# Optimization experiments

Hardware: AMD Instinct MI355X
Metric: run time of the kernel (lower is better)

## Reference

```python
import jax, jax.numpy as jnp
import numpy as np

B, S, D, H = 4, 2048, 1024, 16
HD = D // H
SCALE = HD ** -0.5

def setup_inputs() -> dict:
    key = jax.random.key(0)
    k1, k2, k3 = jax.random.split(key, 3)
    x = jax.random.normal(k1, (B, S, D), dtype=jnp.float32)
    W_qkv = jax.random.normal(k2, (D, 3 * D), dtype=jnp.float32) * (D ** -0.5)
    b_qkv = jnp.zeros((3 * D,), dtype=jnp.float32)
    W_proj = jax.random.normal(k3, (D, D), dtype=jnp.float32) * (D ** -0.5)
    b_proj = jnp.zeros((D,), dtype=jnp.float32)
    return {"x": x, "W_qkv": W_qkv, "b_qkv": b_qkv, "W_proj": W_proj, "b_proj": b_proj}

def reference(x, W_qkv, b_qkv, W_proj, b_proj):
    # x: [B,S,D] -> qkv: [B,S,3D] -> [3,B,H,S,hd]
    qkv = x @ W_qkv + b_qkv
    qkv = qkv.reshape(B, S, 3, H, HD).transpose(2, 0, 3, 1, 4)
    q, k, v = qkv[0], qkv[1], qkv[2]
    # naive full attention: [B,H,S,S]
    attn = jnp.einsum('bhqd,bhkd->bhqk', q, k) * SCALE
    attn = jax.nn.softmax(attn, axis=-1)
    out = jnp.einsum('bhqk,bhkd->bhqd', attn, v)
    out = out.transpose(0, 2, 1, 3).reshape(B, S, D)
    return out @ W_proj + b_proj
```

## Files before the change

### kernel.cpp

```cpp
#include <hip/hip_runtime.h>

typedef __bf16 bf16x8 __attribute__((ext_vector_type(8)));
typedef unsigned short ushort8 __attribute__((ext_vector_type(8)));
typedef float floatx4 __attribute__((ext_vector_type(4)));
typedef unsigned int uintx4 __attribute__((ext_vector_type(4)));

__device__ __forceinline__ unsigned short f2bf(float f) {
  unsigned int u = __builtin_bit_cast(unsigned int, f);
  u += 0x7fffu + ((u >> 16) & 1u);
  return (unsigned short)(u >> 16);
}
__device__ __forceinline__ unsigned int pkbf(float a, float b) {
  unsigned int r;
  asm("v_cvt_pk_bf16_f32 %0, %1, %2" : "=v"(r) : "v"(a), "v"(b));
  return r;
}
__device__ __forceinline__ floatx4 MFMA16(bf16x8 a, bf16x8 b, floatx4 c) {
  return __builtin_amdgcn_mfma_f32_16x16x32_bf16(a, b, c, 0, 0, 0);
}

#define GLOAD16(gsrc, ldst)                                                  \
  __builtin_amdgcn_global_load_lds(                                          \
      (const __attribute__((address_space(1))) void*)(gsrc),                 \
      (__attribute__((address_space(3))) void*)(ldst), 16, 0, 0)

__global__ __launch_bounds__(256) void fill_f32(
    float* __restrict__ out, float val, size_t n) {
  const size_t t = (size_t)blockIdx.x * 256 + threadIdx.x;
  for (size_t i = t; i < n; i += (size_t)gridDim.x * 256) out[i] = val;
}

__global__ __launch_bounds__(256) void cvt_f32_bf16(
    const float* __restrict__ in, unsigned short* __restrict__ out) {
  const size_t t = (size_t)blockIdx.x * 256 + threadIdx.x;
  const float4 a = ((const float4*)in)[2 * t];
  const float4 b = ((const float4*)in)[2 * t + 1];
  uintx4 u;
  u[0] = pkbf(a.x, a.y); u[1] = pkbf(a.z, a.w);
  u[2] = pkbf(b.x, b.y); u[3] = pkbf(b.z, b.w);
  *(uintx4*)&out[t * 8] = u;
}

__global__ __launch_bounds__(256) void transpose_w(
    const float* __restrict__ in, unsigned short* __restrict__ out, int C) {
  __shared__ float T[64][65];
  const int tid = threadIdx.x;
  const int r0 = blockIdx.y * 64, c0 = blockIdx.x * 64;
#pragma unroll
  for (int e = 0; e < 4; ++e) {
    const int idx = e * 256 + tid;
    const int row = idx >> 4, cg = idx & 15;
    const float4 f = *(const float4*)&in[(size_t)(r0 + row) * C + c0 + cg * 4];
    T[row][cg * 4] = f.x; T[row][cg * 4 + 1] = f.y;
    T[row][cg * 4 + 2] = f.z; T[row][cg * 4 + 3] = f.w;
  }
  __syncthreads();
#pragma unroll
  for (int e = 0; e < 2; ++e) {
    const int idx = e * 256 + tid;
    const int cc = idx >> 3, rg = idx & 7;
    uintx4 u;
#pragma unroll
    for (int k = 0; k < 4; ++k)
      u[k] = pkbf(T[rg * 8 + 2 * k][cc], T[rg * 8 + 2 * k + 1][cc]);
    *(uintx4*)&out[(size_t)(c0 + cc) * 1024 + r0 + rg * 8] = u;
  }
}

template <int EPI>
__global__ __launch_bounds__(256) void gemm_nt(
    const unsigned short* __restrict__ A, const unsigned short* __restrict__ Bt,
    const float* __restrict__ bias, unsigned short* __restrict__ o0,
    unsigned short* __restrict__ o1, unsigned short* __restrict__ o2,
    float* __restrict__ of, int M, int N, int K) {
  __shared__ __align__(16) unsigned short As[128 * 32];
  __shared__ __align__(16) unsigned short Bs[128 * 32];
  constexpr int NBX = (EPI == 0) ? 24 : 8;
  constexpr int QX = (NBX * 64) / 8;
  const int tid = threadIdx.x;
  const int lane = tid & 63;
  const int w = tid >> 6;
  const int g = lane >> 4, l15 = lane & 15;
  const int wr = w >> 1, wc = w & 1;
  const int orig = blockIdx.y * NBX + blockIdx.x;
  const int wgid = (orig & 7) * QX + (orig >> 3);
  const int m0 = (wgid / NBX) * 128, n0 = (wgid % NBX) * 128;
  const floatx4 fzero = {0.f, 0.f, 0.f, 0.f};
  floatx4 acc[4][4];
#pragma unroll
  for (int i = 0; i < 4; ++i)
#pragma unroll
    for (int j = 0; j < 4; ++j) acc[i][j] = fzero;

  for (int k0 = 0; k0 < K; k0 += 32) {
#pragma unroll
    for (int p = 0; p < 2; ++p) {
      const int j = p * 256 + tid;
      const int row = j >> 2, cg = j & 3;
      const int dstg = p * 256 + (tid & ~63);
      GLOAD16(&A[(size_t)(m0 + row) * K + k0 + cg * 8], &As[dstg * 8]);
      GLOAD16(&Bt[(size_t)(n0 + row) * K + k0 + cg * 8], &Bs[dstg * 8]);
    }
    __syncthreads();
    bf16x8 af[4], bfr[4];
#pragma unroll
    for (int i = 0; i < 4; ++i)
      af[i] = *(const bf16x8*)&As[(wr * 64 + i * 16 + l15) * 32 + g * 8];
#pragma unroll
    for (int j = 0; j < 4; ++j)
      bfr[j] = *(const bf16x8*)&Bs[(wc * 64 + j * 16 + l15) * 32 + g * 8];
#pragma unroll
    for (int i = 0; i < 4; ++i)
#pragma unroll
      for (int j = 0; j < 4; ++j) acc[i][j] = MFMA16(af[i], bfr[j], acc[i][j]);
    __syncthreads();
  }
#pragma unroll
  for (int i = 0; i < 4; ++i) {
#pragma unroll
    for (int j = 0; j < 4; ++j) {
      const int n = n0 + wc * 64 + j * 16 + l15;
      const float bv = bias[n];
      float vv[4];
#pragma unroll
      for (int r = 0; r < 4; ++r) vv[r] = acc[i][j][r] + bv;
      const int mb = m0 + wr * 64 + i * 16 + g * 4;
      if (EPI == 0) {
        const int three = n >> 10, h = (n >> 6) & 15, hd = n & 63;
        const int b = mb >> 11, s = mb & 2047;
        if (three == 2) {
          ushort4 pk;
          pk.x = f2bf(vv[0]); pk.y = f2bf(vv[1]);
          pk.z = f2bf(vv[2]); pk.w = f2bf(vv[3]);
          const int half = (s >> 5) & 1, hi16 = (s >> 4) & 1, gg = (s >> 2) & 3;
          const int col = (s & ~63) + (half * 4 + gg) * 8 + hi16 * 4;
          *(ushort4*)&o2[(((size_t)(b * 16 + h)) * 64 + hd) * 2048 + col] = pk;
        } else {
          const size_t idx0 = (((size_t)(b * 16 + h)) * 2048 + s) * 64 + hd;
#pragma unroll
          for (int r = 0; r < 4; ++r) {
            if (three == 0)
              o0[idx0 + (size_t)r * 64] = f2bf(vv[r] * 0.1803368801f);
            else
              o1[idx0 + (size_t)r * 64] = f2bf(vv[r]);
          }
        }
      } else {
#pragma unroll
        for (int r = 0; r < 4; ++r) of[(size_t)(mb + r) * N + n] = vv[r];
      }
    }
  }
}

__global__ __launch_bounds__(512) void attn_fwd(
    const unsigned short* __restrict__ Q, const unsigned short* __restrict__ Kq,
    const unsigned short* __restrict__ Vt, unsigned short* __restrict__ Ao) {
  __shared__ __align__(16) unsigned short Ks[2][128 * 64];
  __shared__ __align__(16) unsigned short Vs[2][64 * 128];
  const int bh = blockIdx.y;
  const int tid = threadIdx.x;
  const int lane = tid & 63;
  const int w = tid >> 6;
  const int g = lane >> 4, l15 = lane & 15;
  const int q0 = blockIdx.x * 128 + w * 16;
  const unsigned short* Qp = Q + (size_t)bh * 2048 * 64;
  const unsigned short* Kp = Kq + (size_t)bh * 2048 * 64;
  const unsigned short* Vp = Vt + (size_t)bh * 64 * 2048;

  bf16x8 qf0 = *(const bf16x8*)&Qp[(size_t)(q0 + l15) * 64 + g * 8];
  bf16x8 qf1 = *(const bf16x8*)&Qp[(size_t)(q0 + l15) * 64 + 32 + g * 8];

  const floatx4 minit = {-24.f, -24.f, -24.f, -24.f};
  float lpart = 0.0f;
  floatx4 o[4];
#pragma unroll
  for (int tl = 0; tl < 4; ++tl) o[tl] = {0.f, 0.f, 0.f, 0.f};

  const int x7 = l15 & 7;
  unsigned koffb[2], voff[2];
#pragma unroll
  for (int dh = 0; dh < 2; ++dh)
    koffb[dh] = l15 * 128 + (((dh * 4 + g) ^ x7) * 16);
#pragma unroll
  for (int half = 0; half < 2; ++half)
    voff[half] = l15 * 256 + (((half * 4 + g) ^ x7) * 16);
  const char* ksbase = (const char*)&Ks[0][0];
  const char* vsbase = (const char*)&Vs[0][0];

  const unsigned short* ksrc[2];
  const unsigned short* vsrc[2];
  int dsto[2];
#pragma unroll
  for (int p = 0; p < 2; ++p) {
    const int j = p * 512 + tid;
    const int jsrc = (j & ~7) | ((j & 7) ^ ((j >> 3) & 7));
    ksrc[p] = Kp + jsrc * 8;
    const int vrow = j >> 4, sg = j & 15;
    const int vsg = (sg & 8) | ((sg & 7) ^ (vrow & 7));
    vsrc[p] = Vp + (size_t)vrow * 2048 + vsg * 8;
    dsto[p] = ((j & ~63)) * 8;
  }

#define STAGE(BUF, kv0)                                                       \
  do {                                                                        \
    _Pragma("unroll") for (int p = 0; p < 2; ++p) {                           \
      GLOAD16(ksrc[p] + (size_t)(kv0) * 64, &Ks[BUF][dsto[p]]);               \
      GLOAD16(vsrc[p] + (kv0), &Vs[BUF][dsto[p]]);                            \
    }                                                                         \
  } while (0)

#define COMPUTE(BUF)                                                          \
  do {                                                                        \
    floatx4 s[8];                                                             \
    __builtin_amdgcn_s_setprio(1);                                            \
    _Pragma("unroll") for (int kvf = 0; kvf < 8; ++kvf) {                     \
      bf16x8 kf0 = *(const bf16x8*)(ksbase + (BUF)*16384 + kvf * 2048 +       \
                                    koffb[0]);                                \
      bf16x8 kf1 = *(const bf16x8*)(ksbase + (BUF)*16384 + kvf * 2048 +       \
                                    koffb[1]);                                \
      s[kvf] = MFMA16(kf0, qf0, minit);                                       \
      s[kvf] = MFMA16(kf1, qf1, s[kvf]);                                      \
    }                                                                         \
    __builtin_amdgcn_s_setprio(0);                                            \
    float p[8][4];                                                            \
    _Pragma("unroll") for (int kvf = 0; kvf < 8; ++kvf)                       \
        _Pragma("unroll") for (int r = 0; r < 4; ++r) p[kvf][r] =             \
        exp2f(s[kvf][r]);                                                     \
                                    \
    float t16[16];                                                            \
    _Pragma("unroll") for (int e = 0; e < 16; ++e) t16[e] =                   \
        p[e >> 1][(e & 1) * 2] + p[e >> 1][(e & 1) * 2 + 1];                  \
    float t8[8];                                                              \
    _Pragma("unroll") for (int e = 0; e < 8; ++e) t8[e] =                     \
        t16[2 * e] + t16[2 * e + 1];                                          \
    float t4[4];                                                              \
    _Pragma("unroll") for (int e = 0; e < 4; ++e) t4[e] = t8[2 * e] +         \
        t8[2 * e + 1];                                                        \
    lpart += (t4[0] + t4[1]) + (t4[2] + t4[3]);                               \
    bf16x8 pf[4];                                                             \
    _Pragma("unroll") for (int blk = 0; blk < 4; ++blk) {                     \
      uintx4 wa;                                                              \
      wa[0] = pkbf(p[2 * blk][0], p[2 * blk][1]);                             \
      wa[1] = pkbf(p[2 * blk][2], p[2 * blk][3]);                             \
      wa[2] = pkbf(p[2 * blk + 1][0], p[2 * blk + 1][1]);                     \
      wa[3] = pkbf(p[2 * blk + 1][2], p[2 * blk + 1][3]);                     \
      pf[blk] = __builtin_bit_cast(bf16x8, wa);                               \
    }                                                                         \
    __builtin_amdgcn_s_setprio(1);                                            \
    _Pragma("unroll") for (int tl = 0; tl < 4; ++tl) {                        \
      _Pragma("unroll") for (int blk = 0; blk < 4; ++blk) {                   \
        bf16x8 vf = *(const bf16x8*)(vsbase + (BUF)*16384 + tl * 4096 +       \
                                     (blk >> 1) * 128 + voff[blk & 1]);       \
        o[tl] = MFMA16(pf[blk], vf, o[tl]);                                   \
      }                                                                       \
    }                                                                         \
    __builtin_amdgcn_s_setprio(0);                                            \
  } while (0)

  STAGE(0, 0);
  __syncthreads();
#pragma unroll 1
  for (int t0 = 0; t0 < 16; t0 += 2) {
    STAGE(1, (t0 + 1) * 128);
    COMPUTE(0);
    __syncthreads();
    if (t0 + 2 < 16) STAGE(0, (t0 + 2) * 128);
    COMPUTE(1);
    __syncthreads();
  }
#undef STAGE
#undef COMPUTE

  const int b = bh >> 4, h = bh & 15;
  float l = lpart;
  l += __shfl_xor(l, 16);
  l += __shfl_xor(l, 32);
  const float linv = 1.0f / l;
  float li[4];
#pragma unroll
  for (int r = 0; r < 4; ++r) li[r] = __shfl(linv, (lane & 48) | (g * 4 + r));
#pragma unroll
  for (int tl = 0; tl < 4; ++tl)
#pragma unroll
    for (int r = 0; r < 4; ++r)
      Ao[((size_t)(b * 2048 + q0 + g * 4 + r)) * 1024 + h * 64 + tl * 16 + l15] =
          f2bf(o[tl][r] * li[r]);
}

extern "C" void kernel_launch(void* const* d_in, const int* in_sizes, int n_in,
                              void* d_out, int out_size, void* d_ws, size_t ws_size,
                              hipStream_t stream) {
  float* outf = (float*)d_out;
  const size_t OUTN = (size_t)8192 * 1024;

  const float *x = nullptr, *Wqkv = nullptr, *bqkv = nullptr, *Wproj = nullptr,
              *bproj = nullptr;
  for (int i = 0; i < n_in; ++i) {
    switch (in_sizes[i]) {
      case 8388608: x = (const float*)d_in[i]; break;
      case 3145728: Wqkv = (const float*)d_in[i]; break;
      case 3072:    bqkv = (const float*)d_in[i]; break;
      case 1048576: Wproj = (const float*)d_in[i]; break;
      case 1024:    bproj = (const float*)d_in[i]; break;
      default: break;
    }
  }
  if (!x || !Wqkv || !bqkv || !Wproj || !bproj || n_in != 5) {
    fill_f32<<<2048, 256, 0, stream>>>(outf, 5000.0f, OUTN);
    return;
  }
  const size_t SZ = (size_t)4 * 16 * 2048 * 64 * 2;
  if (ws_size < 3 * SZ) {
    fill_f32<<<2048, 256, 0, stream>>>(outf, 1000.0f + (float)(ws_size >> 20), OUTN);
    return;
  }

  char* ws = (char*)d_ws;
  unsigned short* xb = (unsigned short*)(ws);
  unsigned short* Kb = (unsigned short*)(ws + SZ);
  unsigned short* Vtb = (unsigned short*)(ws + 2 * SZ);
  unsigned short* Qb = (unsigned short*)d_out;
  unsigned short* Wtq = (unsigned short*)((char*)d_out + SZ);
  unsigned short* Ao = xb;
  unsigned short* Wtp = Kb;

  cvt_f32_bf16<<<4096, 256, 0, stream>>>(x, xb);
  transpose_w<<<dim3(48, 16), 256, 0, stream>>>(Wqkv, Wtq, 3072);
  gemm_nt<0><<<dim3(24, 64), 256, 0, stream>>>(
      xb, Wtq, bqkv, Qb, Kb, Vtb, nullptr, 8192, 3072, 1024);
  attn_fwd<<<dim3(16, 64), 512, 0, stream>>>(Qb, Kb, Vtb, Ao);
  transpose_w<<<dim3(16, 16), 256, 0, stream>>>(Wproj, Wtp, 1024);
  gemm_nt<1><<<dim3(8, 64), 256, 0, stream>>>(
      Ao, Wtp, bproj, nullptr, nullptr, nullptr, outf, 8192, 1024, 1024);
}
```

Before: 229.4 us.

## Process two query groups per wave in attention to reuse K/V fragments

New measurement: 228.5 us. About the same (-0.4%).

```diff
diff --git a/kernel.cpp b/kernel.cpp
--- a/kernel.cpp
+++ b/kernel.cpp
@@ -156,35 +156,39 @@
 __global__ __launch_bounds__(512) void attn_fwd(
     const unsigned short* __restrict__ Q, const unsigned short* __restrict__ Kq,
     const unsigned short* __restrict__ Vt, unsigned short* __restrict__ Ao) {
-  __shared__ __align__(16) unsigned short Ks[2][128 * 64];
-  __shared__ __align__(16) unsigned short Vs[2][64 * 128];
+  __shared__ __align__(16) unsigned short Ks[2][8192];
+  __shared__ __align__(16) unsigned short Vs[2][8192];
   const int bh = blockIdx.y;
   const int tid = threadIdx.x;
   const int lane = tid & 63;
   const int w = tid >> 6;
   const int g = lane >> 4, l15 = lane & 15;
-  const int q0 = blockIdx.x * 128 + w * 16;
+  const int q0 = blockIdx.x * 256 + w * 32;
   const unsigned short* Qp = Q + (size_t)bh * 2048 * 64;
   const unsigned short* Kp = Kq + (size_t)bh * 2048 * 64;
   const unsigned short* Vp = Vt + (size_t)bh * 64 * 2048;
 
-  bf16x8 qf0 = *(const bf16x8*)&Qp[(size_t)(q0 + l15) * 64 + g * 8];
-  bf16x8 qf1 = *(const bf16x8*)&Qp[(size_t)(q0 + l15) * 64 + 32 + g * 8];
+  bf16x8 qf[2][2];
+#pragma unroll
+  for (int qg = 0; qg < 2; ++qg)
+#pragma unroll
+    for (int dh = 0; dh < 2; ++dh)
+      qf[qg][dh] =
+          *(const bf16x8*)&Qp[(size_t)(q0 + qg * 16 + l15) * 64 + dh * 32 + g * 8];
 
   const floatx4 minit = {-24.f, -24.f, -24.f, -24.f};
-  float lpart = 0.0f;
-  floatx4 o[4];
-#pragma unroll
-  for (int tl = 0; tl < 4; ++tl) o[tl] = {0.f, 0.f, 0.f, 0.f};
+  float lpart[2] = {0.0f, 0.0f};
+  floatx4 o[2][4];
+#pragma unroll
+  for (int qg = 0; qg < 2; ++qg)
+#pragma unroll
+    for (int tl = 0; tl < 4; ++tl) o[qg][tl] = {0.f, 0.f, 0.f, 0.f};
 
   const int x7 = l15 & 7;
-  unsigned koffb[2], voff[2];
+  unsigned koffb[2];
 #pragma unroll
   for (int dh = 0; dh < 2; ++dh)
     koffb[dh] = l15 * 128 + (((dh * 4 + g) ^ x7) * 16);
-#pragma unroll
-  for (int half = 0; half < 2; ++half)
-    voff[half] = l15 * 256 + (((half * 4 + g) ^ x7) * 16);
   const char* ksbase = (const char*)&Ks[0][0];
   const char* vsbase = (const char*)&Vs[0][0];
 
@@ -196,10 +200,9 @@
     const int j = p * 512 + tid;
     const int jsrc = (j & ~7) | ((j & 7) ^ ((j >> 3) & 7));
     ksrc[p] = Kp + jsrc * 8;
-    const int vrow = j >> 4, sg = j & 15;
-    const int vsg = (sg & 8) | ((sg & 7) ^ (vrow & 7));
-    vsrc[p] = Vp + (size_t)vrow * 2048 + vsg * 8;
-    dsto[p] = ((j & ~63)) * 8;
+    const int hi = j >> 9, vrow = (j >> 3) & 63, sg = j & 7;
+    vsrc[p] = Vp + (size_t)vrow * 2048 + (size_t)(hi * 8 + (sg ^ (vrow & 7))) * 8;
+    dsto[p] = (j & ~63) * 8;
   }
 
 #define STAGE(BUF, kv0)                                                       \
@@ -210,52 +213,49 @@
     }                                                                         \
   } while (0)
 
-#define COMPUTE(BUF)                                                          \
+#define CHUNK(BUF, C)                                                         \
   do {                                                                        \
-    floatx4 s[8];                                                             \
+    floatx4 s[2][2];                                                          \
     __builtin_amdgcn_s_setprio(1);                                            \
-    _Pragma("unroll") for (int kvf = 0; kvf < 8; ++kvf) {                     \
+    _Pragma("unroll") for (int e = 0; e < 2; ++e) {                           \
+      const int kvf = (C)*2 + e;                                              \
       bf16x8 kf0 = *(const bf16x8*)(ksbase + (BUF)*16384 + kvf * 2048 +       \
                                     koffb[0]);                                \
       bf16x8 kf1 = *(const bf16x8*)(ksbase + (BUF)*16384 + kvf * 2048 +       \
                                     koffb[1]);                                \
-      s[kvf] = MFMA16(kf0, qf0, minit);                                       \
-      s[kvf] = MFMA16(kf1, qf1, s[kvf]);                                      \
+      _Pragma("unroll") for (int qg = 0; qg < 2; ++qg) {                      \
+        s[qg][e] = MFMA16(kf0, qf[qg][0], minit);                             \
+        s[qg][e] = MFMA16(kf1, qf[qg][1], s[qg][e]);                          \
+      }                                                                       \
     }                                                                         \
     __builtin_amdgcn_s_setprio(0);                                            \
-    float p[8][4];                                                            \
-    _Pragma("unroll") for (int kvf = 0; kvf < 8; ++kvf)                       \
-        _Pragma("unroll") for (int r = 0; r < 4; ++r) p[kvf][r] =             \
-        exp2f(s[kvf][r]);                                                     \
-                                    \
-    float t16[16];                                                            \
-    _Pragma("unroll") for (int e = 0; e < 16; ++e) t16[e] =                   \
-        p[e >> 1][(e & 1) * 2] + p[e >> 1][(e & 1) * 2 + 1];                  \
-    float t8[8];                                                              \
-    _Pragma("unroll") for (int e = 0; e < 8; ++e) t8[e] =                     \
-        t16[2 * e] + t16[2 * e + 1];                                          \
-    float t4[4];                                                              \
-    _Pragma("unroll") for (int e = 0; e < 4; ++e) t4[e] = t8[2 * e] +         \
-        t8[2 * e + 1];                                                        \
-    lpart += (t4[0] + t4[1]) + (t4[2] + t4[3]);                               \
-    bf16x8 pf[4];                                                             \
-    _Pragma("unroll") for (int blk = 0; blk < 4; ++blk) {                     \
+    bf16x8 pf[2];                                                             \
+    _Pragma("unroll") for (int qg = 0; qg < 2; ++qg) {                        \
+      float p0[4], p1[4];                                                     \
+      _Pragma("unroll") for (int r = 0; r < 4; ++r) {                         \
+        p0[r] = exp2f(s[qg][0][r]);                                           \
+        p1[r] = exp2f(s[qg][1][r]);                                           \
+      }                                                                       \
+      lpart[qg] += ((p0[0] + p0[1]) + (p0[2] + p0[3])) +                      \
+                   ((p1[0] + p1[1]) + (p1[2] + p1[3]));                       \
       uintx4 wa;                                                              \
-      wa[0] = pkbf(p[2 * blk][0], p[2 * blk][1]);                             \
-      wa[1] = pkbf(p[2 * blk][2], p[2 * blk][3]);                             \
-      wa[2] = pkbf(p[2 * blk + 1][0], p[2 * blk + 1][1]);                     \
-      wa[3] = pkbf(p[2 * blk + 1][2], p[2 * blk + 1][3]);                     \
-      pf[blk] = __builtin_bit_cast(bf16x8, wa);                               \
+      wa[0] = pkbf(p0[0], p0[1]); wa[1] = pkbf(p0[2], p0[3]);                 \
+      wa[2] = pkbf(p1[0], p1[1]); wa[3] = pkbf(p1[2], p1[3]);                 \
+      pf[qg] = __builtin_bit_cast(bf16x8, wa);                                \
     }                                                                         \
     __builtin_amdgcn_s_setprio(1);                                            \
     _Pragma("unroll") for (int tl = 0; tl < 4; ++tl) {                        \
-      _Pragma("unroll") for (int blk = 0; blk < 4; ++blk) {                   \
-        bf16x8 vf = *(const bf16x8*)(vsbase + (BUF)*16384 + tl * 4096 +       \
-                                     (blk >> 1) * 128 + voff[blk & 1]);       \
-        o[tl] = MFMA16(pf[blk], vf, o[tl]);                                   \
-      }                                                                       \
+      bf16x8 vf = *(const bf16x8*)(vsbase + (BUF)*16384 + ((C) >> 1) * 8192 + \
+                                   tl * 2048 + koffb[(C)&1]);                 \
+      o[0][tl] = MFMA16(pf[0], vf, o[0][tl]);                                 \
+      o[1][tl] = MFMA16(pf[1], vf, o[1][tl]);                                 \
     }                                                                         \
     __builtin_amdgcn_s_setprio(0);                                            \
+  } while (0)
+
+#define COMPUTE(BUF)                                                          \
+  do {                                                                        \
+    CHUNK(BUF, 0); CHUNK(BUF, 1); CHUNK(BUF, 2); CHUNK(BUF, 3);               \
   } while (0)
 
   STAGE(0, 0);
@@ -270,22 +270,26 @@
     __syncthreads();
   }
 #undef STAGE
+#undef CHUNK
 #undef COMPUTE
 
   const int b = bh >> 4, h = bh & 15;
-  float l = lpart;
-  l += __shfl_xor(l, 16);
-  l += __shfl_xor(l, 32);
-  const float linv = 1.0f / l;
-  float li[4];
-#pragma unroll
-  for (int r = 0; r < 4; ++r) li[r] = __shfl(linv, (lane & 48) | (g * 4 + r));
-#pragma unroll
-  for (int tl = 0; tl < 4; ++tl)
-#pragma unroll
-    for (int r = 0; r < 4; ++r)
-      Ao[((size_t)(b * 2048 + q0 + g * 4 + r)) * 1024 + h * 64 + tl * 16 + l15] =
-          f2bf(o[tl][r] * li[r]);
+#pragma unroll
+  for (int qg = 0; qg < 2; ++qg) {
+    float l = lpart[qg];
+    l += __shfl_xor(l, 16);
+    l += __shfl_xor(l, 32);
+    const float linv = 1.0f / l;
+    float li[4];
+#pragma unroll
+    for (int r = 0; r < 4; ++r) li[r] = __shfl(linv, (lane & 48) | (g * 4 + r));
+#pragma unroll
+    for (int tl = 0; tl < 4; ++tl)
+#pragma unroll
+      for (int r = 0; r < 4; ++r)
+        Ao[((size_t)(b * 2048 + q0 + qg * 16 + g * 4 + r)) * 1024 + h * 64 +
+           tl * 16 + l15] = f2bf(o[qg][tl][r] * li[r]);
+  }
 }
 
 extern "C" void kernel_launch(void* const* d_in, const int* in_sizes, int n_in,
@@ -329,7 +333,7 @@
   transpose_w<<<dim3(48, 16), 256, 0, stream>>>(Wqkv, Wtq, 3072);
   gemm_nt<0><<<dim3(24, 64), 256, 0, stream>>>(
       xb, Wtq, bqkv, Qb, Kb, Vtb, nullptr, 8192, 3072, 1024);
-  attn_fwd<<<dim3(16, 64), 512, 0, stream>>>(Qb, Kb, Vtb, Ao);
+  attn_fwd<<<dim3(8, 64), 512, 0, stream>>>(Qb, Kb, Vtb, Ao);
   transpose_w<<<dim3(16, 16), 256, 0, stream>>>(Wproj, Wtp, 1024);
   gemm_nt<1><<<dim3(8, 64), 256, 0, stream>>>(
       Ao, Wtp, bproj, nullptr, nullptr, nullptr, outf, 8192, 1024, 1024);
```

## Remap attention grid so heads stay on one XCD; relayout V tile in LDS

Applied to the files above, without the earlier changes.

New measurement: 223.6 us. 2.5% less time.

```diff
diff --git a/kernel.cpp b/kernel.cpp
--- a/kernel.cpp
+++ b/kernel.cpp
@@ -156,14 +156,17 @@
 __global__ __launch_bounds__(512) void attn_fwd(
     const unsigned short* __restrict__ Q, const unsigned short* __restrict__ Kq,
     const unsigned short* __restrict__ Vt, unsigned short* __restrict__ Ao) {
-  __shared__ __align__(16) unsigned short Ks[2][128 * 64];
-  __shared__ __align__(16) unsigned short Vs[2][64 * 128];
-  const int bh = blockIdx.y;
+  __shared__ __align__(16) unsigned short Ks[2][8192];
+  __shared__ __align__(16) unsigned short Vs[2][8192];
+  const int blk = blockIdx.x;
+  const int xcd = blk & 7, idx = blk >> 3;
+  const int bh = xcd + 8 * (idx >> 4);
+  const int qt = idx & 15;
   const int tid = threadIdx.x;
   const int lane = tid & 63;
   const int w = tid >> 6;
   const int g = lane >> 4, l15 = lane & 15;
-  const int q0 = blockIdx.x * 128 + w * 16;
+  const int q0 = qt * 128 + w * 16;
   const unsigned short* Qp = Q + (size_t)bh * 2048 * 64;
   const unsigned short* Kp = Kq + (size_t)bh * 2048 * 64;
   const unsigned short* Vp = Vt + (size_t)bh * 64 * 2048;
@@ -178,13 +181,10 @@
   for (int tl = 0; tl < 4; ++tl) o[tl] = {0.f, 0.f, 0.f, 0.f};
 
   const int x7 = l15 & 7;
-  unsigned koffb[2], voff[2];
+  unsigned koffb[2];
 #pragma unroll
   for (int dh = 0; dh < 2; ++dh)
     koffb[dh] = l15 * 128 + (((dh * 4 + g) ^ x7) * 16);
-#pragma unroll
-  for (int half = 0; half < 2; ++half)
-    voff[half] = l15 * 256 + (((half * 4 + g) ^ x7) * 16);
   const char* ksbase = (const char*)&Ks[0][0];
   const char* vsbase = (const char*)&Vs[0][0];
 
@@ -196,10 +196,9 @@
     const int j = p * 512 + tid;
     const int jsrc = (j & ~7) | ((j & 7) ^ ((j >> 3) & 7));
     ksrc[p] = Kp + jsrc * 8;
-    const int vrow = j >> 4, sg = j & 15;
-    const int vsg = (sg & 8) | ((sg & 7) ^ (vrow & 7));
-    vsrc[p] = Vp + (size_t)vrow * 2048 + vsg * 8;
-    dsto[p] = ((j & ~63)) * 8;
+    const int hi = j >> 9, vrow = (j >> 3) & 63, sg = j & 7;
+    vsrc[p] = Vp + (size_t)vrow * 2048 + (size_t)(hi * 8 + (sg ^ (vrow & 7))) * 8;
+    dsto[p] = (j & ~63) * 8;
   }
 
 #define STAGE(BUF, kv0)                                                       \
@@ -227,7 +226,6 @@
     _Pragma("unroll") for (int kvf = 0; kvf < 8; ++kvf)                       \
         _Pragma("unroll") for (int r = 0; r < 4; ++r) p[kvf][r] =             \
         exp2f(s[kvf][r]);                                                     \
-                                    \
     float t16[16];                                                            \
     _Pragma("unroll") for (int e = 0; e < 16; ++e) t16[e] =                   \
         p[e >> 1][(e & 1) * 2] + p[e >> 1][(e & 1) * 2 + 1];                  \
@@ -239,20 +237,21 @@
         t8[2 * e + 1];                                                        \
     lpart += (t4[0] + t4[1]) + (t4[2] + t4[3]);                               \
     bf16x8 pf[4];                                                             \
-    _Pragma("unroll") for (int blk = 0; blk < 4; ++blk) {                     \
+    _Pragma("unroll") for (int blkk = 0; blkk < 4; ++blkk) {                  \
       uintx4 wa;                                                              \
-      wa[0] = pkbf(p[2 * blk][0], p[2 * blk][1]);                             \
-      wa[1] = pkbf(p[2 * blk][2], p[2 * blk][3]);                             \
-      wa[2] = pkbf(p[2 * blk + 1][0], p[2 * blk + 1][1]);                     \
-      wa[3] = pkbf(p[2 * blk + 1][2], p[2 * blk + 1][3]);                     \
-      pf[blk] = __builtin_bit_cast(bf16x8, wa);                               \
+      wa[0] = pkbf(p[2 * blkk][0], p[2 * blkk][1]);                           \
+      wa[1] = pkbf(p[2 * blkk][2], p[2 * blkk][3]);                           \
+      wa[2] = pkbf(p[2 * blkk + 1][0], p[2 * blkk + 1][1]);                   \
+      wa[3] = pkbf(p[2 * blkk + 1][2], p[2 * blkk + 1][3]);                   \
+      pf[blkk] = __builtin_bit_cast(bf16x8, wa);                              \
     }                                                                         \
     __builtin_amdgcn_s_setprio(1);                                            \
     _Pragma("unroll") for (int tl = 0; tl < 4; ++tl) {                        \
-      _Pragma("unroll") for (int blk = 0; blk < 4; ++blk) {                   \
-        bf16x8 vf = *(const bf16x8*)(vsbase + (BUF)*16384 + tl * 4096 +       \
-                                     (blk >> 1) * 128 + voff[blk & 1]);       \
-        o[tl] = MFMA16(pf[blk], vf, o[tl]);                                   \
+      _Pragma("unroll") for (int blkk = 0; blkk < 4; ++blkk) {                \
+        bf16x8 vf = *(const bf16x8*)(vsbase + (BUF)*16384 +                   \
+                                     (blkk >> 1) * 8192 + tl * 2048 +         \
+                                     koffb[blkk & 1]);                        \
+        o[tl] = MFMA16(pf[blkk], vf, o[tl]);                                  \
       }                                                                       \
     }                                                                         \
     __builtin_amdgcn_s_setprio(0);                                            \
@@ -329,7 +328,7 @@
   transpose_w<<<dim3(48, 16), 256, 0, stream>>>(Wqkv, Wtq, 3072);
   gemm_nt<0><<<dim3(24, 64), 256, 0, stream>>>(
       xb, Wtq, bqkv, Qb, Kb, Vtb, nullptr, 8192, 3072, 1024);
-  attn_fwd<<<dim3(16, 64), 512, 0, stream>>>(Qb, Kb, Vtb, Ao);
+  attn_fwd<<<1024, 512, 0, stream>>>(Qb, Kb, Vtb, Ao);
   transpose_w<<<dim3(16, 16), 256, 0, stream>>>(Wproj, Wtp, 1024);
   gemm_nt<1><<<dim3(8, 64), 256, 0, stream>>>(
       Ao, Wtp, bproj, nullptr, nullptr, nullptr, outf, 8192, 1024, 1024);
```
